# Optimization experiments

Hardware: AMD Instinct MI355X
Metric: run time of the kernel (lower is better)

## Reference

```python
import jax, jax.numpy as jnp
import numpy as np
from jax import lax

EQN, GR = 10, 4
N, C, H, W = 8, 64, 16, 16


def _build_a(h, w):
    num = h * w
    a = np.zeros((num, EQN, 4 * num), np.float32)
    for i in range(num):
        right = (i + 1) % w != 0 and i + 1 < num
        down = i + w < num
        if right:
            a[i, 0, 2 * num + i] = 1.0; a[i, 0, i + 1] = -1.0
            a[i, 2, 2 * num + i] = 1.0; a[i, 2, 2 * num + i + 1] = -1.0
            a[i, 4, i] = 1.0;           a[i, 4, i + 1] = -1.0
            a[i, 6, 3 * num + i] = 1.0; a[i, 6, 3 * num + i + 1] = -1.0
            a[i, 8, num + i] = 1.0;     a[i, 8, num + i + 1] = -1.0
        if down:
            a[i, 1, 3 * num + i] = 1.0; a[i, 1, num + i + w] = -1.0
            a[i, 3, 3 * num + i] = 1.0; a[i, 3, 3 * num + i + w] = -1.0
            a[i, 5, num + i] = 1.0;     a[i, 5, num + i + w] = -1.0
            a[i, 7, 2 * num + i] = 1.0; a[i, 7, 2 * num + i + w] = -1.0
            a[i, 9, i] = 1.0;           a[i, 9, i + w] = -1.0
    last = num - 1
    a[last, 0, 2 * num + last] = 1.0
    a[last, 1, 3 * num + last] = 1.0
    a[last, 2, 2 * num + last] = 1.0
    a[last, 3, 3 * num + last] = 1.0
    a[last, 4, last] = 1.0
    a[last, 5, num + last] = 1.0
    a[last, 6, 3 * num + last] = 1.0
    a[last, 7, 2 * num + last] = 1.0
    a[last, 8, num + last] = 1.0
    a[last, 9, last] = 1.0
    return jnp.asarray(a)


def _conv(x, w, b):
    y = lax.conv_general_dilated(x, w, (1, 1), 'SAME',
                                 dimension_numbers=('NCHW', 'OIHW', 'NCHW'))
    return y + b[None, :, None, None]


def _lrelu(v):
    return jnp.where(v >= 0, v, 0.01 * v)


def setup_inputs() -> dict:
    key = jax.random.key(0)
    ks = jax.random.split(key, 18)
    s = 0.05
    d = {
        'x':   jax.random.normal(ks[0], (N, C, H, W), jnp.float32),
        'a':   _build_a(H, W),
        'gw1': jax.random.normal(ks[1], (C, C, 3, 3), jnp.float32) * s,
        'gb1': jnp.zeros((C,), jnp.float32),
        'gw2': jax.random.normal(ks[2], (EQN * GR, C, 3, 3), jnp.float32) * s,
        'gb2': jnp.zeros((EQN * GR,), jnp.float32),
        'aw1': jax.random.normal(ks[3], (C, C, 3, 3), jnp.float32) * s,
        'ab1': jnp.zeros((C,), jnp.float32),
        'aw2': jax.random.normal(ks[4], (EQN * GR, C, 3, 3), jnp.float32) * s,
        'ab2': jnp.zeros((EQN * GR,), jnp.float32),
        'sw1': jax.random.normal(ks[5], (C // 2, C, 1, 1), jnp.float32) * s,
        'sb1': jnp.zeros((C // 2,), jnp.float32),
        'sw2': jax.random.normal(ks[6], (4 * GR, C // 2, 1, 1), jnp.float32) * s,
        'sb2': jnp.zeros((4 * GR,), jnp.float32),
        'ins_w': jnp.ones((4 * GR,), jnp.float32),
        'ins_b': jnp.zeros((4 * GR,), jnp.float32),
        'pw':  jax.random.normal(ks[7], (128, 4 * GR, 3, 3), jnp.float32) * s,
        'pb':  jnp.zeros((128,), jnp.float32),
    }
    return d


def reference(x, a, gw1, gb1, gw2, gb2, aw1, ab1, aw2, ab2,
              sw1, sb1, sw2, sb2, ins_w, ins_b, pw, pb):
    n, c, h, w = x.shape
    num = h * w
    # attention / gradient / squeeze-excite branches
    att = jax.nn.sigmoid(_conv(_lrelu(_conv(x, aw1, ab1)), aw2, ab2))   # (n, eqn*gr, h, w)
    g   = _conv(_lrelu(_conv(x, gw1, gb1)), gw2, gb2)                   # (n, eqn*gr, h, w)
    pooled = x.mean(axis=(2, 3), keepdims=True)
    se = jax.nn.sigmoid(_conv(_lrelu(_conv(pooled, sw1, sb1)), sw2, sb2))  # (n, 4*gr, 1, 1)
    # reshape channels (gr, eqn), flatten batch*group, move pixel axis first
    att_r = att.reshape(n * GR, EQN, num).transpose(0, 2, 1)   # (ng, num, eqn)
    g_r   = g.reshape(n * GR, EQN, num).transpose(0, 2, 1)
    # weighted flow-equation system (done for all ng at once; the torch chunked
    # loop is only a memory optimization, math is identical)
    A = (a[None] * att_r[..., None]).reshape(n * GR, num * EQN, 4 * num)
    B = (g_r * att_r).reshape(n * GR, num * EQN)
    ATA = jnp.einsum('bki,bkj->bij', A, A)          # (ng, 4num, 4num)
    ATB = jnp.einsum('bki,bk->bi', A, B)            # (ng, 4num)
    ATA = ATA + jnp.eye(4 * num, dtype=x.dtype) * 1e-12
    sol = jnp.linalg.solve(ATA, ATB[..., None])     # (ng, 4num, 1)
    y = sol.reshape(n, 4 * GR, h, w)
    # GroupNorm(1, 4*gr): normalize over (C,H,W) per sample, per-channel affine
    mu = y.mean(axis=(1, 2, 3), keepdims=True)
    var = ((y - mu) ** 2).mean(axis=(1, 2, 3), keepdims=True)
    y = (y - mu) / jnp.sqrt(var + 1e-5)
    y = y * ins_w[None, :, None, None] + ins_b[None, :, None, None]
    y = se * y
    return _conv(y, pw, pb)
```

## Files before the change

kernel.cpp:

```cpp
#include <hip/hip_runtime.h>
#include <hip/hip_bf16.h>


#define NIT 64

__global__ __launch_bounds__(256) void k_se(
    const float* __restrict__ x, const float* __restrict__ sw1,
    const float* __restrict__ sb1, const float* __restrict__ sw2,
    const float* __restrict__ sb2, float* __restrict__ se)
{
  int n = blockIdx.x, t = threadIdx.x;
  __shared__ float part[64*4];
  __shared__ float pooled[64];
  __shared__ float h1[32];
  int c = t >> 2, q = t & 3;
  const float* xp = x + ((n*64 + c)*256) + q*64;
  float s = 0.f;
  #pragma unroll 8
  for (int j = 0; j < 64; ++j) s += xp[j];
  part[c*4+q] = s;
  __syncthreads();
  if (t < 64) pooled[t] = (part[t*4+0]+part[t*4+1]+part[t*4+2]+part[t*4+3]) * (1.f/256.f);
  __syncthreads();
  if (t < 32) {
    float a = sb1[t];
    for (int c2 = 0; c2 < 64; ++c2) a = fmaf(sw1[t*64+c2], pooled[c2], a);
    h1[t] = a >= 0.f ? a : 0.01f*a;
  }
  __syncthreads();
  if (t < 16) {
    float a = sb2[t];
    for (int c2 = 0; c2 < 32; ++c2) a = fmaf(sw2[t*32+c2], h1[c2], a);
    se[n*16+t] = 1.f/(1.f+__expf(-a));
  }
}

template<int CO_T, int CO_TOTAL, int ACT>
__global__ __launch_bounds__(1024) void k_convw(
    const float* __restrict__ xg, const float* __restrict__ xa,
    const float* __restrict__ wg, const float* __restrict__ bg,
    const float* __restrict__ wa, const float* __restrict__ ba,
    float* __restrict__ outg, float* __restrict__ outa)
{
  const int tiles = CO_TOTAL / CO_T;
  int b = blockIdx.x;
  int tile = b % tiles; int rem = b / tiles;
  int br = rem & 1;     int n = rem >> 1;
  const float* xin  = br ? xa : xg;
  const float* w    = br ? wa : wg;
  const float* bias = br ? ba : bg;
  float* outp       = br ? outa : outg;
  int co_base = tile * CO_T;
  int t = threadIdx.x;
  int pix = t & 255, qc = t >> 8;
  int pr = pix >> 4, pc = pix & 15;
  __shared__ float xs[64*324];
  __shared__ float wl[CO_T*64*12];
  __shared__ float part[3][CO_T][256];
  const float* xn = xin + (size_t)n*64*256;
  for (int idx = t; idx < 64*324; idx += 1024) {
    int ch = idx / 324;
    int rm = idx - ch*324;
    int rr = rm / 18, cc = rm - rr*18;
    int sr = rr - 1, sc = cc - 1;
    float v = 0.f;
    if ((unsigned)sr < 16u && (unsigned)sc < 16u)
      v = xn[ch*256 + sr*16 + sc];
    xs[idx] = v;
  }
  for (int idx = t; idx < CO_T*576; idx += 1024) {
    int co = idx / 576; int rm = idx - co*576;
    int ci = rm / 9; int k = rm - ci*9;
    wl[(co*64 + ci)*12 + k] = w[(size_t)(co_base+co)*576 + rm];
  }
  __syncthreads();
  float accA[CO_T], accB[CO_T];
  #pragma unroll
  for (int co = 0; co < CO_T; ++co) { accA[co] = 0.f; accB[co] = 0.f; }
  int cib = qc*16;
  for (int ci = 0; ci < 8; ++ci) {
    const float* xrA = xs + (cib+ci)*324 + pr*18 + pc;
    const float* xrB = xs + (cib+ci+8)*324 + pr*18 + pc;
    float a0 = xrA[0],  a1 = xrA[1],  a2 = xrA[2];
    float a3 = xrA[18], a4 = xrA[19], a5 = xrA[20];
    float a6 = xrA[36], a7 = xrA[37], a8 = xrA[38];
    float b0 = xrB[0],  b1 = xrB[1],  b2 = xrB[2];
    float b3 = xrB[18], b4 = xrB[19], b5 = xrB[20];
    float b6 = xrB[36], b7 = xrB[37], b8 = xrB[38];
    #pragma unroll
    for (int co = 0; co < CO_T; ++co) {
      const float4* wvA = ((const float4*)wl) + (co*64 + cib+ci)*3;
      const float4* wvB = ((const float4*)wl) + (co*64 + cib+ci+8)*3;
      float4 wa4 = wvA[0], wb4 = wvA[1], wc4 = wvA[2];
      float4 wd4 = wvB[0], we4 = wvB[1], wf4 = wvB[2];
      float aA = accA[co];
      aA = fmaf(a0,wa4.x,aA); aA = fmaf(a1,wa4.y,aA); aA = fmaf(a2,wa4.z,aA);
      aA = fmaf(a3,wa4.w,aA); aA = fmaf(a4,wb4.x,aA); aA = fmaf(a5,wb4.y,aA);
      aA = fmaf(a6,wb4.z,aA); aA = fmaf(a7,wb4.w,aA); aA = fmaf(a8,wc4.x,aA);
      accA[co] = aA;
      float aB = accB[co];
      aB = fmaf(b0,wd4.x,aB); aB = fmaf(b1,wd4.y,aB); aB = fmaf(b2,wd4.z,aB);
      aB = fmaf(b3,wd4.w,aB); aB = fmaf(b4,we4.x,aB); aB = fmaf(b5,we4.y,aB);
      aB = fmaf(b6,we4.z,aB); aB = fmaf(b7,we4.w,aB); aB = fmaf(b8,wf4.x,aB);
      accB[co] = aB;
    }
  }
  if (qc > 0) {
    #pragma unroll
    for (int co = 0; co < CO_T; ++co) part[qc-1][co][pix] = accA[co] + accB[co];
  }
  __syncthreads();
  if (qc == 0) {
    float* ob = outp + ((size_t)n*CO_TOTAL + co_base)*256 + pix;
    #pragma unroll
    for (int co = 0; co < CO_T; ++co) {
      float v = bias[co_base+co] + accA[co] + accB[co] + part[0][co][pix]
              + part[1][co][pix] + part[2][co][pix];
      if (ACT == 1) v = v >= 0.f ? v : 0.01f*v;
      if (ACT == 2 && br) v = 1.f/(1.f+__expf(-v));
      ob[co*256] = v;
    }
  }
}

__device__ __forceinline__ float wave_sum(float x){
  x += __int_as_float(__builtin_amdgcn_update_dpp(0, __float_as_int(x), 0x111, 0xf, 0xf, true));
  x += __int_as_float(__builtin_amdgcn_update_dpp(0, __float_as_int(x), 0x112, 0xf, 0xf, true));
  x += __int_as_float(__builtin_amdgcn_update_dpp(0, __float_as_int(x), 0x114, 0xf, 0xf, true));
  x += __int_as_float(__builtin_amdgcn_update_dpp(0, __float_as_int(x), 0x118, 0xf, 0xf, true));
  x += __int_as_float(__builtin_amdgcn_update_dpp(0, __float_as_int(x), 0x142, 0xa, 0xf, true));
  x += __int_as_float(__builtin_amdgcn_update_dpp(0, __float_as_int(x), 0x143, 0xc, 0xf, true));
  return __int_as_float(__builtin_amdgcn_readlane(__float_as_int(x), 63));
}
__device__ __forceinline__ float dpp_prev(float v){
  return __int_as_float(__builtin_amdgcn_update_dpp(0, __float_as_int(v), 0x138, 0xf, 0xf, true));
}
__device__ __forceinline__ float dpp_next(float v){
  return __int_as_float(__builtin_amdgcn_update_dpp(0, __float_as_int(v), 0x130, 0xf, 0xf, true));
}

__global__ __launch_bounds__(64, 1) void k_cg(
    const float* __restrict__ att, const float* __restrict__ gm,
    float* __restrict__ yout)
{
  int bg = blockIdx.x;
  int n = bg >> 2, g = bg & 3;
  const float* ab = att + ((size_t)n*40 + g*10)*256;
  const float* gb = gm  + ((size_t)n*40 + g*10)*256;
  __shared__ float sbuf[10][256];
  __shared__ float tbuf[10][256];
  __shared__ float pl[4][256];
  int l = threadIdx.x;
  int base = l*4;
  int rI = l >> 2;
  int c0 = (l & 3)*4;
  bool rU4 = (rI > 0), hD4 = (rI < 15);
  int iL0 = (base > 0) ? base-1 : 0;
  int iUc = rU4 ? base-16 : base;
  int iDc = hD4 ? base+16 : base;

  float sr[10][4], tr[10][4];
  #pragma unroll
  for (int e = 0; e < 10; ++e) {
    float4 av = *(const float4*)(ab + e*256 + base);
    float4 gv = *(const float4*)(gb + e*256 + base);
    sr[e][0]=av.x*av.x; sr[e][1]=av.y*av.y; sr[e][2]=av.z*av.z; sr[e][3]=av.w*av.w;
    tr[e][0]=sr[e][0]*gv.x; tr[e][1]=sr[e][1]*gv.y; tr[e][2]=sr[e][2]*gv.z; tr[e][3]=sr[e][3]*gv.w;
    *(float4*)(&sbuf[e][base]) = make_float4(sr[e][0],sr[e][1],sr[e][2],sr[e][3]);
    *(float4*)(&tbuf[e][base]) = make_float4(tr[e][0],tr[e][1],tr[e][2],tr[e][3]);
  }
  __syncthreads();

  const int eL[5] = {0,2,4,6,8};
  const int eU[5] = {1,3,5,7,9};
  float sLs[5][4], tLs[5][4], sUs[5][4], tUs[5][4];
  float gU = rU4 ? 1.f : 0.f;
  #pragma unroll
  for (int k = 0; k < 5; ++k) {
    int e = eL[k];
    sLs[k][0] = (c0 > 0) ? sbuf[e][iL0] : 0.f;
    tLs[k][0] = (c0 > 0) ? tbuf[e][iL0] : 0.f;
    #pragma unroll
    for (int j = 1; j < 4; ++j) { sLs[k][j] = sr[e][j-1]; tLs[k][j] = tr[e][j-1]; }
  }
  #pragma unroll
  for (int k = 0; k < 5; ++k) {
    int e = eU[k];
    float4 su = *(const float4*)(&sbuf[e][iUc]);
    float4 tu = *(const float4*)(&tbuf[e][iUc]);
    sUs[k][0]=su.x*gU; sUs[k][1]=su.y*gU; sUs[k][2]=su.z*gU; sUs[k][3]=su.w*gU;
    tUs[k][0]=tu.x*gU; tUs[k][1]=tu.y*gU; tUs[k][2]=tu.z*gU; tUs[k][3]=tu.w*gU;
  }

  float k0R[4],k0L[4],k0X[4],k0D[4],k0U[4], d0[4],di0[4], b0[4];
  float k1R[4],k1L[4],k1D[4],k1U[4],k1X[4], d1[4],di1[4], b1[4];
  float k2R[4],k2L[4],k2D[4],k2U[4],k2X[4], d2[4],di2[4], b2[4];
  float k3R[4],k3L[4],k3D[4],k3U[4],k3X[4], d3[4],di3[4], b3[4];
  #pragma unroll
  for (int j = 0; j < 4; ++j) {
    bool hR = (c0 + j) < 15;
    bool hD = hD4;
    bool last = (l == 63) && (j == 3);
    k0R[j] = hR ? sr[4][j] : 0.f;  k0L[j] = sLs[2][j];  k0X[j] = sLs[0][j];
    k0D[j] = hD ? sr[9][j] : 0.f;  k0U[j] = sUs[4][j];
    k1R[j] = hR ? sr[8][j] : 0.f;  k1L[j] = sLs[4][j];
    k1D[j] = hD ? sr[5][j] : 0.f;  k1U[j] = sUs[2][j];  k1X[j] = sUs[0][j];
    k2R[j] = hR ? sr[2][j] : 0.f;  k2L[j] = sLs[1][j];
    k2D[j] = hD ? sr[7][j] : 0.f;  k2U[j] = sUs[3][j];  k2X[j] = hR ? sr[0][j] : 0.f;
    k3R[j] = hR ? sr[6][j] : 0.f;  k3L[j] = sLs[3][j];
    k3D[j] = hD ? sr[3][j] : 0.f;  k3U[j] = sUs[1][j];  k3X[j] = hD ? sr[1][j] : 0.f;
    d0[j] = k0R[j]+k0L[j]+k0X[j]+k0D[j]+k0U[j] + (last ? sr[4][j]+sr[9][j] : 0.f);
    d1[j] = k1R[j]+k1L[j]+k1D[j]+k1U[j]+k1X[j] + (last ? sr[5][j]+sr[8][j] : 0.f);
    d2[j] = k2R[j]+k2L[j]+k2D[j]+k2U[j]+k2X[j] + (last ? sr[0][j]+sr[2][j]+sr[7][j] : 0.f);
    d3[j] = k3R[j]+k3L[j]+k3D[j]+k3U[j]+k3X[j] + (last ? sr[1][j]+sr[3][j]+sr[6][j] : 0.f);
    b0[j] = (hR?tr[4][j]:0.f) - tLs[2][j] - tLs[0][j] + (hD?tr[9][j]:0.f) - tUs[4][j]
          + (last ? tr[4][j]+tr[9][j] : 0.f);
    b1[j] = (hR?tr[8][j]:0.f) - tLs[4][j] + (hD?tr[5][j]:0.f) - tUs[2][j] - tUs[0][j]
          + (last ? tr[5][j]+tr[8][j] : 0.f);
    b2[j] = (hR?(tr[2][j]+tr[0][j]):0.f) - tLs[1][j] + (hD?tr[7][j]:0.f) - tUs[3][j]
          + (last ? tr[0][j]+tr[2][j]+tr[7][j] : 0.f);
    b3[j] = (hR?tr[6][j]:0.f) - tLs[3][j] + (hD?(tr[3][j]+tr[1][j]):0.f) - tUs[1][j]
          + (last ? tr[1][j]+tr[3][j]+tr[6][j] : 0.f);
    di0[j] = 1.f/(d0[j]+1e-20f); di1[j] = 1.f/(d1[j]+1e-20f);
    di2[j] = 1.f/(d2[j]+1e-20f); di3[j] = 1.f/(d3[j]+1e-20f);
  }

  float vA = sr[0][3]+sr[2][3]+sr[4][3]+sr[7][3]+sr[9][3];
  float vB = sr[1][3]+sr[3][3]+sr[5][3]+sr[6][3]+sr[8][3];
  float ei1 = 1.f/(__shfl(vA, 63, 64)+1e-20f);
  float ei2 = 1.f/(__shfl(vB, 63, 64)+1e-20f);

  float x0[4],x1[4],x2[4],x3[4], r0[4],r1[4],r2[4],r3[4], p0[4],p1[4],p2[4],p3[4];
  float rdr_p = 0.f, ca_p = 0.f, cb_p = 0.f;
  #pragma unroll
  for (int j = 0; j < 4; ++j) {
    x0[j]=0.f; x1[j]=0.f; x2[j]=0.f; x3[j]=0.f;
    r0[j]=b0[j]; r1[j]=b1[j]; r2[j]=b2[j]; r3[j]=b3[j];
    rdr_p += r0[j]*r0[j]*di0[j] + r1[j]*r1[j]*di1[j] + r2[j]*r2[j]*di2[j] + r3[j]*r3[j]*di3[j];
    ca_p += r0[j]+r2[j]; cb_p += r1[j]+r3[j];
  }
  float rdr = wave_sum(rdr_p), ca = wave_sum(ca_p), cb = wave_sum(cb_p);
  float rz = rdr + ca*ca*ei1 + cb*cb*ei2;
  float cc1 = ca*ei1, cc2 = cb*ei2;
  #pragma unroll
  for (int j = 0; j < 4; ++j) {
    p0[j] = di0[j]*r0[j] + cc1; p1[j] = di1[j]*r1[j] + cc2;
    p2[j] = di2[j]*r2[j] + cc1; p3[j] = di3[j]*r3[j] + cc2;
  }
  *(float4*)(&pl[0][base]) = make_float4(p0[0],p0[1],p0[2],p0[3]);
  *(float4*)(&pl[1][base]) = make_float4(p1[0],p1[1],p1[2],p1[3]);
  *(float4*)(&pl[2][base]) = make_float4(p2[0],p2[1],p2[2],p2[3]);
  *(float4*)(&pl[3][base]) = make_float4(p3[0],p3[1],p3[2],p3[3]);
  __syncthreads();

  for (int it = 0; it < NIT; ++it) {
    float nR0 = dpp_next(p0[0]), nR1 = dpp_next(p1[0]),
          nR2 = dpp_next(p2[0]), nR3 = dpp_next(p3[0]);
    float nL0 = dpp_prev(p0[3]), nL1 = dpp_prev(p1[3]),
          nL2 = dpp_prev(p2[3]), nL3 = dpp_prev(p3[3]);
    float4 u0 = *(const float4*)(&pl[0][iUc]);
    float4 u1 = *(const float4*)(&pl[1][iUc]);
    float4 u2 = *(const float4*)(&pl[2][iUc]);
    float4 u3 = *(const float4*)(&pl[3][iUc]);
    float4 w0 = *(const float4*)(&pl[0][iDc]);
    float4 w1 = *(const float4*)(&pl[1][iDc]);
    float4 w2 = *(const float4*)(&pl[2][iDc]);
    float4 w3 = *(const float4*)(&pl[3][iDc]);
    float pU0[4]={u0.x,u0.y,u0.z,u0.w}, pU1[4]={u1.x,u1.y,u1.z,u1.w};
    float pU2[4]={u2.x,u2.y,u2.z,u2.w}, pU3[4]={u3.x,u3.y,u3.z,u3.w};
    float pD0[4]={w0.x,w0.y,w0.z,w0.w}, pD1[4]={w1.x,w1.y,w1.z,w1.w};
    float pD2[4]={w2.x,w2.y,w2.z,w2.w}, pD3[4]={w3.x,w3.y,w3.z,w3.w};
    float q0[4],q1[4],q2[4],q3[4];
    float pq_p = 0.f;
    #pragma unroll
    for (int j = 0; j < 4; ++j) {
      float p0R = (j<3)? p0[j+1] : nR0;  float p0L = (j>0)? p0[j-1] : nL0;
      float p1R = (j<3)? p1[j+1] : nR1;  float p1L = (j>0)? p1[j-1] : nL1;
      float p2R = (j<3)? p2[j+1] : nR2;  float p2L = (j>0)? p2[j-1] : nL2;
      float p3R = (j<3)? p3[j+1] : nR3;  float p3L = (j>0)? p3[j-1] : nL3;
      q0[j] = d0[j]*p0[j] - k0R[j]*p0R - k0L[j]*p0L - k0X[j]*p2L - k0D[j]*pD0[j] - k0U[j]*pU0[j];
      q1[j] = d1[j]*p1[j] - k1R[j]*p1R - k1L[j]*p1L - k1D[j]*pD1[j] - k1U[j]*pU1[j] - k1X[j]*pU3[j];
      q2[j] = d2[j]*p2[j] - k2R[j]*p2R - k2L[j]*p2L - k2D[j]*pD2[j] - k2U[j]*pU2[j] - k2X[j]*p0R;
      q3[j] = d3[j]*p3[j] - k3R[j]*p3R - k3L[j]*p3L - k3D[j]*pD3[j] - k3U[j]*pU3[j] - k3X[j]*pD1[j];
      pq_p += p0[j]*q0[j] + p1[j]*q1[j] + p2[j]*q2[j] + p3[j]*q3[j];
    }
    float pq = wave_sum(pq_p);
    float alpha = pq > 1e-35f ? rz/pq : 0.f;
    float rdr2_p = 0.f, ca2_p = 0.f, cb2_p = 0.f;
    #pragma unroll
    for (int j = 0; j < 4; ++j) {
      x0[j] = fmaf(alpha,p0[j],x0[j]); x1[j] = fmaf(alpha,p1[j],x1[j]);
      x2[j] = fmaf(alpha,p2[j],x2[j]); x3[j] = fmaf(alpha,p3[j],x3[j]);
      r0[j] = fmaf(-alpha,q0[j],r0[j]); r1[j] = fmaf(-alpha,q1[j],r1[j]);
      r2[j] = fmaf(-alpha,q2[j],r2[j]); r3[j] = fmaf(-alpha,q3[j],r3[j]);
      rdr2_p += r0[j]*r0[j]*di0[j] + r1[j]*r1[j]*di1[j] + r2[j]*r2[j]*di2[j] + r3[j]*r3[j]*di3[j];
      ca2_p += r0[j]+r2[j]; cb2_p += r1[j]+r3[j];
    }
    float rdrT = wave_sum(rdr2_p), c1T = wave_sum(ca2_p), c2T = wave_sum(cb2_p);
    float rz2 = rdrT + c1T*c1T*ei1 + c2T*c2T*ei2;
    float beta = rz > 1e-35f ? rz2/rz : 0.f;
    rz = rz2;
    float z1c = c1T*ei1, z2c = c2T*ei2;
    #pragma unroll
    for (int j = 0; j < 4; ++j) {
      p0[j] = fmaf(beta,p0[j], di0[j]*r0[j] + z1c);
      p1[j] = fmaf(beta,p1[j], di1[j]*r1[j] + z2c);
      p2[j] = fmaf(beta,p2[j], di2[j]*r2[j] + z1c);
      p3[j] = fmaf(beta,p3[j], di3[j]*r3[j] + z2c);
    }
    *(float4*)(&pl[0][base]) = make_float4(p0[0],p0[1],p0[2],p0[3]);
    *(float4*)(&pl[1][base]) = make_float4(p1[0],p1[1],p1[2],p1[3]);
    *(float4*)(&pl[2][base]) = make_float4(p2[0],p2[1],p2[2],p2[3]);
    *(float4*)(&pl[3][base]) = make_float4(p3[0],p3[1],p3[2],p3[3]);
    __syncthreads();
  }
  float* yo = yout + ((size_t)n*16 + g*4)*256 + base;
  *(float4*)(yo)       = make_float4(x0[0],x0[1],x0[2],x0[3]);
  *(float4*)(yo + 256) = make_float4(x1[0],x1[1],x1[2],x1[3]);
  *(float4*)(yo + 512) = make_float4(x2[0],x2[1],x2[2],x2[3]);
  *(float4*)(yo + 768) = make_float4(x3[0],x3[1],x3[2],x3[3]);
}

template<int CO_T>
__global__ __launch_bounds__(256) void k_out(
    const float* __restrict__ y, const float* __restrict__ insw,
    const float* __restrict__ insb, const float* __restrict__ sev,
    const float* __restrict__ pw, const float* __restrict__ pb,
    float* __restrict__ out)
{
  const int tiles = 128 / CO_T;
  int b = blockIdx.x;
  int cot = b % tiles, n = b / tiles;
  int co_base = cot * CO_T;
  int t = threadIdx.x;
  int pr = t >> 4, pc = t & 15;
  __shared__ float ys[16*324];
  __shared__ float wl[CO_T*16*12];
  __shared__ float redA[4], redB[4];
  const float* yb = y + (size_t)n*16*256;
  float s = 0.f, s2 = 0.f;
  #pragma unroll
  for (int c = 0; c < 16; ++c) {
    float v = yb[c*256 + t];
    s += v; s2 = fmaf(v, v, s2);
  }
  for (int idx = t; idx < CO_T*144; idx += 256) {
    int co = idx / 144; int rm = idx - co*144;
    int ci = rm / 9; int k = rm - ci*9;
    wl[(co*16 + ci)*12 + k] = pw[(size_t)(co_base+co)*144 + rm];
  }
  for (int idx = t; idx < 16*324; idx += 256) {
    int ch = idx / 324;
    int rem = idx - ch*324;
    int rr = rem / 18, cc = rem - rr*18;
    int sr = rr-1, sc = cc-1;
    float v = 0.f;
    if ((unsigned)sr < 16u && (unsigned)sc < 16u) v = yb[ch*256 + sr*16 + sc];
    ys[idx] = v;
  }
  int lane = t & 63, wid = t >> 6;
  #pragma unroll
  for (int m = 1; m < 64; m <<= 1) { s += __shfl_xor(s, m, 64); s2 += __shfl_xor(s2, m, 64); }
  if (lane == 0) { redA[wid] = s; redB[wid] = s2; }
  __syncthreads();
  float S  = redA[0]+redA[1]+redA[2]+redA[3];
  float SS = redB[0]+redB[1]+redB[2]+redB[3];
  float mu = S * (1.f/4096.f);
  float var = SS * (1.f/4096.f) - mu*mu;
  float rstd = rsqrtf(var + 1e-5f);
  for (int idx = t; idx < 16*324; idx += 256) {
    int ch = idx / 324;
    int rem = idx - ch*324;
    int rr = rem / 18, cc = rem - rr*18;
    int sr = rr-1, sc = cc-1;
    if ((unsigned)sr < 16u && (unsigned)sc < 16u) {
      float sef = sev[n*16+ch];
      float m = rstd * insw[ch] * sef;
      float a = (insb[ch] - mu*rstd*insw[ch]) * sef;
      ys[idx] = fmaf(ys[idx], m, a);
    }
  }
  __syncthreads();
  float acc[CO_T];
  #pragma unroll
  for (int co = 0; co < CO_T; ++co) acc[co] = pb[co_base+co];
  for (int ci = 0; ci < 16; ++ci) {
    const float* xr = ys + ci*324 + pr*18 + pc;
    float x0 = xr[0],  x1 = xr[1],  x2 = xr[2];
    float x3 = xr[18], x4 = xr[19], x5 = xr[20];
    float x6 = xr[36], x7 = xr[37], x8 = xr[38];
    #pragma unroll
    for (int co = 0; co < CO_T; ++co) {
      const float4* wv = ((const float4*)wl) + (co*16 + ci)*3;
      float4 wa = wv[0], wb = wv[1], wc = wv[2];
      float a = acc[co];
      a = fmaf(x0,wa.x,a); a = fmaf(x1,wa.y,a); a = fmaf(x2,wa.z,a);
      a = fmaf(x3,wa.w,a); a = fmaf(x4,wb.x,a); a = fmaf(x5,wb.y,a);
      a = fmaf(x6,wb.z,a); a = fmaf(x7,wb.w,a); a = fmaf(x8,wc.x,a);
      acc[co] = a;
    }
  }
  float* ob = out + ((size_t)n*128 + co_base)*256 + t;
  #pragma unroll
  for (int co = 0; co < CO_T; ++co)
    ob[co*256] = acc[co];
}

extern "C" void kernel_launch(void* const* d_in, const int* in_sizes, int n_in,
                              void* d_out, int out_size, void* d_ws, size_t ws_size,
                              hipStream_t stream) {
  const float* x    = (const float*)d_in[0];
  const float* gw1  = (const float*)d_in[2];
  const float* gb1  = (const float*)d_in[3];
  const float* gw2  = (const float*)d_in[4];
  const float* gb2  = (const float*)d_in[5];
  const float* aw1  = (const float*)d_in[6];
  const float* ab1  = (const float*)d_in[7];
  const float* aw2  = (const float*)d_in[8];
  const float* ab2  = (const float*)d_in[9];
  const float* sw1  = (const float*)d_in[10];
  const float* sb1  = (const float*)d_in[11];
  const float* sw2  = (const float*)d_in[12];
  const float* sb2  = (const float*)d_in[13];
  const float* insw = (const float*)d_in[14];
  const float* insb = (const float*)d_in[15];
  const float* pw   = (const float*)d_in[16];
  const float* pb   = (const float*)d_in[17];
  float* ws = (float*)d_ws;
  float* g1   = ws;
  float* a1   = ws + 131072;
  float* gmat = ws + 262144;
  float* attb = ws + 344064;
  float* sev  = ws + 425984;
  float* ybuf = ws + 426112;
  float* out  = (float*)d_out;

  k_se<<<dim3(8), dim3(256), 0, stream>>>(x, sw1, sb1, sw2, sb2, sev);
  k_convw<4,64,1><<<dim3(256), dim3(1024), 0, stream>>>(x, x, gw1, gb1, aw1, ab1, g1, a1);
  k_convw<4,40,2><<<dim3(160), dim3(1024), 0, stream>>>(g1, a1, gw2, gb2, aw2, ab2, gmat, attb);
  k_cg<<<dim3(32), dim3(64), 0, stream>>>(attb, gmat, ybuf);
  k_out<4><<<dim3(256), dim3(256), 0, stream>>>(ybuf, insw, insb, sev, pw, pb, out);
}
```

Measured before the change: 95.44 us.

## Hold conv weights in registers and broadcast them with readlane instead of LDS

The conv kernel no longer stages weights in shared memory. Each lane loads the weights for one input channel into registers, and the inner loop fetches each weight with v_readlane into a scalar register. This removes the LDS weight buffer and its ds_read traffic, and lowers shared memory use. In exchange it costs CO_T*9 extra VGPRs per thread and many readlane instructions, which may limit occupancy with 1024-thread blocks.

```diff
diff --git a/kernel.cpp b/kernel.cpp
--- a/kernel.cpp
+++ b/kernel.cpp
@@ -33,6 +33,10 @@
     for (int c2 = 0; c2 < 32; ++c2) a = fmaf(sw2[t*32+c2], h1[c2], a);
     se[n*16+t] = 1.f/(1.f+__expf(-a));
   }
+}
+
+__device__ __forceinline__ float lane_bcast(float v, int src){
+  return __int_as_float(__builtin_amdgcn_readlane(__float_as_int(v), src));
 }
 
 template<int CO_T, int CO_TOTAL, int ACT>
@@ -54,9 +58,18 @@
   int t = threadIdx.x;
   int pix = t & 255, qc = t >> 8;
   int pr = pix >> 4, pc = pix & 15;
+  int lane = t & 63;
+  int cib = qc*16;
   __shared__ float xs[64*324];
-  __shared__ float wl[CO_T*64*12];
   __shared__ float part[3][CO_T][256];
+  int cil = cib + (lane & 15);
+  float wv[CO_T*9];
+  #pragma unroll
+  for (int co = 0; co < CO_T; ++co) {
+    const float* wp = w + ((size_t)(co_base+co)*64 + cil)*9;
+    #pragma unroll
+    for (int k = 0; k < 9; ++k) wv[co*9+k] = wp[k];
+  }
   const float* xn = xin + (size_t)n*64*256;
   for (int idx = t; idx < 64*324; idx += 1024) {
     int ch = idx / 324;
@@ -68,16 +81,11 @@
       v = xn[ch*256 + sr*16 + sc];
     xs[idx] = v;
   }
-  for (int idx = t; idx < CO_T*576; idx += 1024) {
-    int co = idx / 576; int rm = idx - co*576;
-    int ci = rm / 9; int k = rm - ci*9;
-    wl[(co*64 + ci)*12 + k] = w[(size_t)(co_base+co)*576 + rm];
-  }
   __syncthreads();
   float accA[CO_T], accB[CO_T];
   #pragma unroll
   for (int co = 0; co < CO_T; ++co) { accA[co] = 0.f; accB[co] = 0.f; }
-  int cib = qc*16;
+  #pragma unroll
   for (int ci = 0; ci < 8; ++ci) {
     const float* xrA = xs + (cib+ci)*324 + pr*18 + pc;
     const float* xrB = xs + (cib+ci+8)*324 + pr*18 + pc;
@@ -89,19 +97,27 @@
     float b6 = xrB[36], b7 = xrB[37], b8 = xrB[38];
     #pragma unroll
     for (int co = 0; co < CO_T; ++co) {
-      const float4* wvA = ((const float4*)wl) + (co*64 + cib+ci)*3;
-      const float4* wvB = ((const float4*)wl) + (co*64 + cib+ci+8)*3;
-      float4 wa4 = wvA[0], wb4 = wvA[1], wc4 = wvA[2];
-      float4 wd4 = wvB[0], we4 = wvB[1], wf4 = wvB[2];
       float aA = accA[co];
-      aA = fmaf(a0,wa4.x,aA); aA = fmaf(a1,wa4.y,aA); aA = fmaf(a2,wa4.z,aA);
-      aA = fmaf(a3,wa4.w,aA); aA = fmaf(a4,wb4.x,aA); aA = fmaf(a5,wb4.y,aA);
-      aA = fmaf(a6,wb4.z,aA); aA = fmaf(a7,wb4.w,aA); aA = fmaf(a8,wc4.x,aA);
+      aA = fmaf(a0, lane_bcast(wv[co*9+0], ci), aA);
+      aA = fmaf(a1, lane_bcast(wv[co*9+1], ci), aA);
+      aA = fmaf(a2, lane_bcast(wv[co*9+2], ci), aA);
+      aA = fmaf(a3, lane_bcast(wv[co*9+3], ci), aA);
+      aA = fmaf(a4, lane_bcast(wv[co*9+4], ci), aA);
+      aA = fmaf(a5, lane_bcast(wv[co*9+5], ci), aA);
+      aA = fmaf(a6, lane_bcast(wv[co*9+6], ci), aA);
+      aA = fmaf(a7, lane_bcast(wv[co*9+7], ci), aA);
+      aA = fmaf(a8, lane_bcast(wv[co*9+8], ci), aA);
       accA[co] = aA;
       float aB = accB[co];
-      aB = fmaf(b0,wd4.x,aB); aB = fmaf(b1,wd4.y,aB); aB = fmaf(b2,wd4.z,aB);
-      aB = fmaf(b3,wd4.w,aB); aB = fmaf(b4,we4.x,aB); aB = fmaf(b5,we4.y,aB);
-      aB = fmaf(b6,we4.z,aB); aB = fmaf(b7,we4.w,aB); aB = fmaf(b8,wf4.x,aB);
+      aB = fmaf(b0, lane_bcast(wv[co*9+0], ci+8), aB);
+      aB = fmaf(b1, lane_bcast(wv[co*9+1], ci+8), aB);
+      aB = fmaf(b2, lane_bcast(wv[co*9+2], ci+8), aB);
+      aB = fmaf(b3, lane_bcast(wv[co*9+3], ci+8), aB);
+      aB = fmaf(b4, lane_bcast(wv[co*9+4], ci+8), aB);
+      aB = fmaf(b5, lane_bcast(wv[co*9+5], ci+8), aB);
+      aB = fmaf(b6, lane_bcast(wv[co*9+6], ci+8), aB);
+      aB = fmaf(b7, lane_bcast(wv[co*9+7], ci+8), aB);
+      aB = fmaf(b8, lane_bcast(wv[co*9+8], ci+8), aB);
       accB[co] = aB;
     }
   }
```

Measured after the change: 93.21 us. 2.3% less time.
